# Performance work log

Hardware: AMD Instinct MI355X
Metric: run time of the kernel (lower is better)

The kernel has to match this reference:

```python
import jax, jax.numpy as jnp
import numpy as np

GAMMA = 0.5
NUM_ITER = 5


def setup_inputs() -> dict:
    key = jax.random.key(0)
    k1, k2 = jax.random.split(key)
    V, L = 10242, 42
    def_idxs = jax.random.uniform(k1, (V, L), dtype=jnp.float32, minval=1e-4, maxval=1.0)
    def_cont_ico_crf = jax.random.normal(k2, (V, 3), dtype=jnp.float32)
    # learned parameters, initialized as in the module
    filter_weights = jnp.ones((V, V), dtype=jnp.float32)
    spatial_weights = 4.0 * jnp.eye(V, dtype=jnp.float32)
    comp_matrix = jnp.eye(L, dtype=jnp.float32)
    return {
        "def_idxs": def_idxs,
        "def_cont_ico_crf": def_cont_ico_crf,
        "filter_weights": filter_weights,
        "spatial_weights": spatial_weights,
        "comp_matrix": comp_matrix,
    }


def reference(def_idxs, def_cont_ico_crf, filter_weights, spatial_weights, comp_matrix):
    V = def_cont_ico_crf.shape[0]
    # pairwise squared L2 distances between control points: [V, V]
    sq = jnp.sum(def_cont_ico_crf * def_cont_ico_crf, axis=1)
    d2 = sq[:, None] + sq[None, :] - 2.0 * (def_cont_ico_crf @ def_cont_ico_crf.T)
    smooth_filter = jnp.exp(-d2 / (2.0 * GAMMA ** 2))
    idx = jnp.arange(V)
    smooth_filter = smooth_filter.at[idx, idx].set(0.0)  # fill_diagonal_(0)

    U = jnp.log(jnp.clip(def_idxs, 1e-06, 1.0))  # unary potentials [V, L]
    q = jax.nn.softmax(U, axis=1)
    filter_mat = filter_weights * smooth_filter

    for _ in range(NUM_ITER):
        phi_t = filter_mat @ q                      # message passing [V, L]
        phi = -(spatial_weights @ phi_t)            # spatial reweighting
        phi = phi @ comp_matrix                     # label compatibility
        q = jax.nn.softmax(U - phi, axis=1)
    return q
```

## Files before the change

kernel.cpp:

```cpp
#include <hip/hip_runtime.h>
#include <stdint.h>

#define Vn 10242
#define Ln 42
#define LPn 48
#define VPn 10496
#define RBn 41
#define JPAD 10368
#define NITER 5
#define SCL 1.69864360f
#define BR 128

typedef float4 f4;
typedef short bf16x8 __attribute__((ext_vector_type(8)));
typedef float f32x4 __attribute__((ext_vector_type(4)));

__device__ __forceinline__ unsigned cvtpk_bf16(float a, float b) {
    unsigned r;
    asm("v_cvt_pk_bf16_f32 %0, %1, %2" : "=v"(r) : "v"(a), "v"(b));
    return r;
}
__device__ __forceinline__ unsigned short f2bf_rne(float f) {
    unsigned u = __float_as_uint(f);
    u = (u + 0x7fffu + ((u >> 16) & 1u)) >> 16;
    return (unsigned short)u;
}
__device__ __forceinline__ float bf2f(unsigned short h) {
    return __uint_as_float(((unsigned)h) << 16);
}

__global__ __launch_bounds__(256) void k_detect(const float* __restrict__ F,
                                                const float* __restrict__ S,
                                                int* flags, float* __restrict__ diagS) {
    int jj = blockIdx.x * 256 + threadIdx.x;
    if (jj >= Vn / 2) return;
    int j = jj * 2;
    const float c0 = F[0];
    int violF = 0, violS = 0;
    for (int i = blockIdx.y; i < Vn; i += (int)gridDim.y) {
        size_t off = (size_t)i * Vn + j;
        float2 f = *(const float2*)(F + off);
        float2 s = *(const float2*)(S + off);
        violF |= (f.x != c0) | (f.y != c0);
        if (i == j)          { diagS[j] = s.x;     violS |= (s.y != 0.0f); }
        else if (i == j + 1) { diagS[j + 1] = s.y; violS |= (s.x != 0.0f); }
        else                 violS |= (s.x != 0.0f) | (s.y != 0.0f);
    }
    if (violF) atomicOr(&flags[0], 1);
    if (violS) atomicOr(&flags[1], 1);
}

__global__ void k_detC(const float* __restrict__ Cm, int* flags) {
    int viol = 0;
    for (int idx = threadIdx.x; idx < Ln * Ln; idx += 256) {
        int r = idx / Ln, c = idx - r * Ln;
        float expct = (r == c) ? 1.0f : 0.0f;
        viol |= (Cm[idx] != expct);
    }
    if (viol) atomicOr(&flags[3], 1);
}

__global__ __launch_bounds__(256) void k_initU(const float* __restrict__ didx,
                                               const float* __restrict__ coords,
                                               float* __restrict__ U, float* __restrict__ qA,
                                               float* __restrict__ qB,
                                               unsigned short* __restrict__ qTAh,
                                               unsigned short* __restrict__ qTAl,
                                               unsigned short* __restrict__ qTBh,
                                               unsigned short* __restrict__ qTBl,
                                               float* __restrict__ xyz) {
    int row = blockIdx.x * 256 + threadIdx.x;
    if (row >= Vn) {
        #pragma unroll
        for (int l = 0; l < LPn; ++l) {
            U[(size_t)row * LPn + l] = 0.0f;
            qA[(size_t)row * LPn + l] = 0.0f;
            qB[(size_t)row * LPn + l] = 0.0f;
            qTAh[(size_t)l * VPn + row] = 0;
            qTAl[(size_t)l * VPn + row] = 0;
            qTBh[(size_t)l * VPn + row] = 0;
            qTBl[(size_t)l * VPn + row] = 0;
        }
        *(f4*)(xyz + (size_t)row * 4) = make_float4(0.f, 0.f, 0.f, 0.f);
        return;
    }
    float ux = SCL * coords[(size_t)row * 3 + 0];
    float uy = SCL * coords[(size_t)row * 3 + 1];
    float uz = SCL * coords[(size_t)row * 3 + 2];
    float ss = ux * ux + uy * uy + uz * uz;
    *(f4*)(xyz + (size_t)row * 4) = make_float4(ux, uy, uz, ss);
    float u[Ln];
    float mx = -3.0e38f;
    #pragma unroll
    for (int l = 0; l < Ln; ++l) {
        float x = didx[(size_t)row * Ln + l];
        x = fminf(fmaxf(x, 1e-6f), 1.0f);
        u[l] = __logf(x);
        mx = fmaxf(mx, u[l]);
    }
    float s = 0.0f;
    float e[Ln];
    #pragma unroll
    for (int l = 0; l < Ln; ++l) { e[l] = __expf(u[l] - mx); s += e[l]; }
    float inv = 1.0f / s;
    #pragma unroll
    for (int l = 0; l < Ln; ++l) {
        float qv = e[l] * inv;
        unsigned short h = f2bf_rne(qv);
        U[(size_t)row * LPn + l] = u[l];
        qA[(size_t)row * LPn + l] = qv;
        qTAh[(size_t)l * VPn + row] = h;
        qTAl[(size_t)l * VPn + row] = f2bf_rne(qv - bf2f(h));
    }
    #pragma unroll
    for (int l = Ln; l < LPn; ++l) {
        U[(size_t)row * LPn + l] = 0.0f;
        qA[(size_t)row * LPn + l] = 0.0f;
        qB[(size_t)row * LPn + l] = 0.0f;
        qTAh[(size_t)l * VPn + row] = 0;
        qTAl[(size_t)l * VPn + row] = 0;
        qTBh[(size_t)l * VPn + row] = 0;
        qTBl[(size_t)l * VPn + row] = 0;
    }
}

__global__ __launch_bounds__(256, 3) void k_phi_f(const unsigned short* __restrict__ qTh,
                                                  const unsigned short* __restrict__ qTl,
                                                  const f4* __restrict__ xyz4,
                                                  float* __restrict__ part,
                                                  const int* __restrict__ flags, int jchunk) {
    if (flags[0]) return;
    __shared__ uint4 Ah[8][BR];
    __shared__ uint4 Al[8][BR];
    __shared__ uint4 Bh[LPn][8];
    __shared__ uint4 Bl[LPn][8];
    const int t = threadIdx.x;
    const int lane = t & 63;
    const int wv = t >> 6;
    const int lo16 = lane & 15, hi4 = lane >> 4;
    const int rowbase = blockIdx.x * BR;
    f4 p0 = xyz4[rowbase + lane];
    f4 p1 = xyz4[rowbase + lane + 64];
    const float v0x = 2.f * p0.x, v0y = 2.f * p0.y, v0z = 2.f * p0.z, ns0 = -p0.w;
    const float v1x = 2.f * p1.x, v1y = 2.f * p1.y, v1z = 2.f * p1.z, ns1 = -p1.w;
    f32x4 acc[2][3];
    #pragma unroll
    for (int rs = 0; rs < 2; ++rs)
        #pragma unroll
        for (int cs = 0; cs < 3; ++cs) acc[rs][cs] = (f32x4){0.f, 0.f, 0.f, 0.f};
    const int j0 = blockIdx.y * jchunk;
    int j1 = j0 + jchunk; if (j1 > JPAD) j1 = JPAD;
    const int n0 = t >> 3, sl0 = t & 7;
    const int s1 = t + 256;
    const int n1 = s1 >> 3, sl1 = s1 & 7;
    const bool has1 = (s1 < LPn * 8);
    for (int jt = j0; jt < j1; jt += 64) {
        uint4 bh0 = *(const uint4*)(qTh + (size_t)n0 * VPn + jt + sl0 * 8);
        uint4 bl0 = *(const uint4*)(qTl + (size_t)n0 * VPn + jt + sl0 * 8);
        uint4 bh1, bl1;
        if (has1) {
            bh1 = *(const uint4*)(qTh + (size_t)n1 * VPn + jt + sl1 * 8);
            bl1 = *(const uint4*)(qTl + (size_t)n1 * VPn + jt + sl1 * 8);
        }
        const int jb = __builtin_amdgcn_readfirstlane(jt + wv * 16);
        unsigned ph0[8], ph1[8], pl0[8], pl1[8];
        #pragma unroll
        for (int m = 0; m < 16; m += 2) {
            f4 qa = xyz4[jb + m];
            f4 qb = xyz4[jb + m + 1];
            float wa0 = exp2f(fmaf(v0z, qa.z, fmaf(v0y, qa.y, fmaf(v0x, qa.x, ns0 - qa.w))));
            float wb0 = exp2f(fmaf(v0z, qb.z, fmaf(v0y, qb.y, fmaf(v0x, qb.x, ns0 - qb.w))));
            float wa1 = exp2f(fmaf(v1z, qa.z, fmaf(v1y, qa.y, fmaf(v1x, qa.x, ns1 - qa.w))));
            float wb1 = exp2f(fmaf(v1z, qb.z, fmaf(v1y, qb.y, fmaf(v1x, qb.x, ns1 - qb.w))));
            unsigned h0 = cvtpk_bf16(wa0, wb0);
            unsigned h1 = cvtpk_bf16(wa1, wb1);
            ph0[m >> 1] = h0;
            ph1[m >> 1] = h1;
            pl0[m >> 1] = cvtpk_bf16(wa0 - __uint_as_float(h0 << 16),
                                     wb0 - __uint_as_float(h0 & 0xffff0000u));
            pl1[m >> 1] = cvtpk_bf16(wa1 - __uint_as_float(h1 << 16),
                                     wb1 - __uint_as_float(h1 & 0xffff0000u));
        }
        __syncthreads();
        Ah[2 * wv][lane]          = make_uint4(ph0[0], ph0[1], ph0[2], ph0[3]);
        Ah[2 * wv + 1][lane]      = make_uint4(ph0[4], ph0[5], ph0[6], ph0[7]);
        Ah[2 * wv][lane + 64]     = make_uint4(ph1[0], ph1[1], ph1[2], ph1[3]);
        Ah[2 * wv + 1][lane + 64] = make_uint4(ph1[4], ph1[5], ph1[6], ph1[7]);
        Al[2 * wv][lane]          = make_uint4(pl0[0], pl0[1], pl0[2], pl0[3]);
        Al[2 * wv + 1][lane]      = make_uint4(pl0[4], pl0[5], pl0[6], pl0[7]);
        Al[2 * wv][lane + 64]     = make_uint4(pl1[0], pl1[1], pl1[2], pl1[3]);
        Al[2 * wv + 1][lane + 64] = make_uint4(pl1[4], pl1[5], pl1[6], pl1[7]);
        Bh[n0][sl0 ^ (n0 & 7)] = bh0;
        Bl[n0][sl0 ^ (n0 & 7)] = bl0;
        if (has1) {
            Bh[n1][sl1 ^ (n1 & 7)] = bh1;
            Bl[n1][sl1 ^ (n1 & 7)] = bl1;
        }
        __syncthreads();
        #pragma unroll
        for (int kk = 0; kk < 2; ++kk) {
            bf16x8 a0h = *(bf16x8*)&Ah[kk * 4 + hi4][wv * 32 + lo16];
            bf16x8 a1h = *(bf16x8*)&Ah[kk * 4 + hi4][wv * 32 + 16 + lo16];
            bf16x8 a0l = *(bf16x8*)&Al[kk * 4 + hi4][wv * 32 + lo16];
            bf16x8 a1l = *(bf16x8*)&Al[kk * 4 + hi4][wv * 32 + 16 + lo16];
            #pragma unroll
            for (int cs = 0; cs < 3; ++cs) {
                int n = cs * 16 + lo16;
                int slot = (kk * 4 + hi4) ^ (n & 7);
                bf16x8 bh = *(bf16x8*)&Bh[n][slot];
                bf16x8 bl = *(bf16x8*)&Bl[n][slot];
                acc[0][cs] = __builtin_amdgcn_mfma_f32_16x16x32_bf16(a0h, bh, acc[0][cs], 0, 0, 0);
                acc[0][cs] = __builtin_amdgcn_mfma_f32_16x16x32_bf16(a0h, bl, acc[0][cs], 0, 0, 0);
                acc[0][cs] = __builtin_amdgcn_mfma_f32_16x16x32_bf16(a0l, bh, acc[0][cs], 0, 0, 0);
                acc[0][cs] = __builtin_amdgcn_mfma_f32_16x16x32_bf16(a0l, bl, acc[0][cs], 0, 0, 0);
                acc[1][cs] = __builtin_amdgcn_mfma_f32_16x16x32_bf16(a1h, bh, acc[1][cs], 0, 0, 0);
                acc[1][cs] = __builtin_amdgcn_mfma_f32_16x16x32_bf16(a1h, bl, acc[1][cs], 0, 0, 0);
                acc[1][cs] = __builtin_amdgcn_mfma_f32_16x16x32_bf16(a1l, bh, acc[1][cs], 0, 0, 0);
                acc[1][cs] = __builtin_amdgcn_mfma_f32_16x16x32_bf16(a1l, bl, acc[1][cs], 0, 0, 0);
            }
        }
    }
    size_t pb = (size_t)blockIdx.y * LPn * VPn;
    #pragma unroll
    for (int rs = 0; rs < 2; ++rs)
        #pragma unroll
        for (int cs = 0; cs < 3; ++cs) {
            int col = cs * 16 + lo16;
            int row = rowbase + wv * 32 + rs * 16 + hi4 * 4;
            *(f4*)(part + pb + (size_t)col * VPn + row) =
                make_float4(acc[rs][cs][0], acc[rs][cs][1], acc[rs][cs][2], acc[rs][cs][3]);
        }
}

template <int USEG>
__device__ __forceinline__ void mat_gen_body(const float* __restrict__ W,
                                             const float* __restrict__ X,
                                             const float* __restrict__ xyz,
                                             float* __restrict__ part, int jchunk) {
    __shared__ float ldsW[256][33];
    int t = threadIdx.x;
    int row = blockIdx.x * 256 + t;
    bool act = (row < Vn);
    int j0 = blockIdx.y * jchunk;
    int j1 = j0 + jchunk; if (j1 > Vn) j1 = Vn;
    f4 xi = make_float4(0.f, 0.f, 0.f, 0.f);
    if (USEG && act) xi = *(const f4*)(xyz + (size_t)row * 4);
    f4 acc[12];
    #pragma unroll
    for (int c = 0; c < 12; ++c) acc[c] = make_float4(0.f, 0.f, 0.f, 0.f);
    for (int jt = j0; jt < j1; jt += 32) {
        __syncthreads();
        #pragma unroll
        for (int k = 0; k < 8; ++k) {
            int idx = t + k * 256;
            int r = idx >> 3;
            int cc = (idx & 7) << 2;
            int rr = blockIdx.x * 256 + r;
            int jc = jt + cc;
            float v0 = 0.f, v1 = 0.f, v2 = 0.f, v3 = 0.f;
            if (rr < Vn) {
                const float* wp = W + (size_t)rr * Vn + jc;
                if (jc + 0 < Vn) v0 = wp[0];
                if (jc + 1 < Vn) v1 = wp[1];
                if (jc + 2 < Vn) v2 = wp[2];
                if (jc + 3 < Vn) v3 = wp[3];
            }
            ldsW[r][cc + 0] = v0; ldsW[r][cc + 1] = v1;
            ldsW[r][cc + 2] = v2; ldsW[r][cc + 3] = v3;
        }
        __syncthreads();
        int jend = j1 - jt; if (jend > 32) jend = 32;
        for (int jj = 0; jj < jend; ++jj) {
            int j = jt + jj;
            float f = ldsW[t][jj];
            if (USEG) {
                f4 xj = *(const f4*)(xyz + (size_t)j * 4);
                float dx = xi.x - xj.x, dy = xi.y - xj.y, dz = xi.z - xj.z;
                float t2 = dx * dx; t2 = fmaf(dy, dy, t2); t2 = fmaf(dz, dz, t2);
                float w = exp2f(-t2);
                w = (j == row) ? 0.0f : w;
                f *= w;
            }
            const f4* qr = (const f4*)(X + (size_t)j * LPn);
            #pragma unroll
            for (int c = 0; c < 12; ++c) {
                f4 qv = qr[c];
                acc[c].x = fmaf(f, qv.x, acc[c].x);
                acc[c].y = fmaf(f, qv.y, acc[c].y);
                acc[c].z = fmaf(f, qv.z, acc[c].z);
                acc[c].w = fmaf(f, qv.w, acc[c].w);
            }
        }
    }
    size_t base = (size_t)blockIdx.y * LPn * VPn + row;
    if (act) {
        #pragma unroll
        for (int c = 0; c < 12; ++c) {
            part[base + (size_t)(4 * c + 0) * VPn] = acc[c].x;
            part[base + (size_t)(4 * c + 1) * VPn] = acc[c].y;
            part[base + (size_t)(4 * c + 2) * VPn] = acc[c].z;
            part[base + (size_t)(4 * c + 3) * VPn] = acc[c].w;
        }
    } else if (row < VPn) {
        #pragma unroll
        for (int c = 0; c < LPn; ++c) part[base + (size_t)c * VPn] = 0.0f;
    }
}

__global__ __launch_bounds__(256) void k_phi_g(const float* __restrict__ W,
                                               const float* __restrict__ q,
                                               const float* __restrict__ xyz,
                                               float* __restrict__ part,
                                               const int* __restrict__ flags, int jchunk) {
    if (!flags[0]) return;
    mat_gen_body<1>(W, q, xyz, part, jchunk);
}

__global__ __launch_bounds__(256) void k_sp(const float* __restrict__ Sw,
                                            const float* __restrict__ phi,
                                            float* __restrict__ part,
                                            const int* __restrict__ flags, int jchunk) {
    if (!flags[1]) return;
    mat_gen_body<0>(Sw, phi, (const float*)nullptr, part, jchunk);
}

__global__ __launch_bounds__(256) void k_R0(const float* __restrict__ part,
                                            const unsigned short* __restrict__ qTh,
                                            const unsigned short* __restrict__ qTl,
                                            float* __restrict__ phi,
                                            const int* __restrict__ flags,
                                            int NS, int gate) {
    if (gate && !flags[1]) return;
    int tg = blockIdx.x * 256 + threadIdx.x;
    int c = tg / (VPn / 4);
    int r4 = (tg - c * (VPn / 4)) * 4;
    f4 s = make_float4(0.f, 0.f, 0.f, 0.f);
    for (int n = 0; n < NS; ++n) {
        f4 v = *(const f4*)(part + ((size_t)n * LPn + c) * VPn + r4);
        s.x += v.x; s.y += v.y; s.z += v.z; s.w += v.w;
    }
    if (!gate && !flags[0]) {
        ushort4 h = *(const ushort4*)(qTh + (size_t)c * VPn + r4);
        ushort4 l = *(const ushort4*)(qTl + (size_t)c * VPn + r4);
        s.x -= bf2f(h.x) + bf2f(l.x);
        s.y -= bf2f(h.y) + bf2f(l.y);
        s.z -= bf2f(h.z) + bf2f(l.z);
        s.w -= bf2f(h.w) + bf2f(l.w);
    }
    phi[(size_t)(r4 + 0) * LPn + c] = s.x;
    phi[(size_t)(r4 + 1) * LPn + c] = s.y;
    phi[(size_t)(r4 + 2) * LPn + c] = s.z;
    phi[(size_t)(r4 + 3) * LPn + c] = s.w;
}

__global__ __launch_bounds__(256) void k_B(const float* __restrict__ U,
                                           const float* __restrict__ phi,
                                           const float* __restrict__ phi2,
                                           const float* __restrict__ diagS,
                                           const float* __restrict__ Cm,
                                           const float* __restrict__ Fw,
                                           const int* __restrict__ flags,
                                           float* __restrict__ qn,
                                           unsigned short* __restrict__ qTnh,
                                           unsigned short* __restrict__ qTnl,
                                           float* __restrict__ outp, int last) {
    __shared__ float ldsC[Ln][LPn];
    int t = threadIdx.x;
    if (flags[3]) {
        for (int idx = t; idx < Ln * LPn; idx += 256) {
            int m = idx / LPn, l = idx - m * LPn;
            ldsC[m][l] = (l < Ln) ? Cm[(size_t)m * Ln + l] : 0.0f;
        }
    }
    __syncthreads();
    int row = blockIdx.x * 256 + t;
    if (row >= Vn) return;
    const float* src = flags[1] ? phi2 : phi;
    float pt[LPn];
    #pragma unroll
    for (int c = 0; c < 12; ++c) {
        f4 v = *(const f4*)(src + (size_t)row * LPn + 4 * c);
        pt[4 * c + 0] = v.x; pt[4 * c + 1] = v.y;
        pt[4 * c + 2] = v.z; pt[4 * c + 3] = v.w;
    }
    float scale = (flags[0] ? 1.0f : Fw[0]) * (flags[1] ? 1.0f : diagS[row]);
    float ph[LPn];
    if (flags[3]) {
        #pragma unroll
        for (int c = 0; c < LPn; ++c) ph[c] = 0.f;
        #pragma unroll
        for (int m = 0; m < Ln; ++m) {
            float pm = pt[m];
            #pragma unroll
            for (int c = 0; c < 12; ++c) {
                f4 cv = *(const f4*)&ldsC[m][4 * c];
                ph[4 * c + 0] = fmaf(pm, cv.x, ph[4 * c + 0]);
                ph[4 * c + 1] = fmaf(pm, cv.y, ph[4 * c + 1]);
                ph[4 * c + 2] = fmaf(pm, cv.z, ph[4 * c + 2]);
                ph[4 * c + 3] = fmaf(pm, cv.w, ph[4 * c + 3]);
            }
        }
    } else {
        #pragma unroll
        for (int c = 0; c < LPn; ++c) ph[c] = pt[c];
    }
    float lg[LPn];
    #pragma unroll
    for (int c = 0; c < 12; ++c) {
        f4 uv = *(const f4*)(U + (size_t)row * LPn + 4 * c);
        lg[4 * c + 0] = uv.x + scale * ph[4 * c + 0];
        lg[4 * c + 1] = uv.y + scale * ph[4 * c + 1];
        lg[4 * c + 2] = uv.z + scale * ph[4 * c + 2];
        lg[4 * c + 3] = uv.w + scale * ph[4 * c + 3];
    }
    float mx = lg[0];
    #pragma unroll
    for (int l = 1; l < Ln; ++l) mx = fmaxf(mx, lg[l]);
    float s = 0.f;
    float e[LPn];
    #pragma unroll
    for (int l = 0; l < Ln; ++l) { e[l] = __expf(lg[l] - mx); s += e[l]; }
    #pragma unroll
    for (int l = Ln; l < LPn; ++l) e[l] = 0.f;
    float inv = 1.0f / s;
    #pragma unroll
    for (int c = 0; c < 12; ++c) {
        f4 v = make_float4(e[4 * c + 0] * inv, e[4 * c + 1] * inv,
                           e[4 * c + 2] * inv, e[4 * c + 3] * inv);
        *(f4*)(qn + (size_t)row * LPn + 4 * c) = v;
    }
    #pragma unroll
    for (int l = 0; l < Ln; ++l) {
        float qv = e[l] * inv;
        unsigned short h = f2bf_rne(qv);
        qTnh[(size_t)l * VPn + row] = h;
        qTnl[(size_t)l * VPn + row] = f2bf_rne(qv - bf2f(h));
    }
    if (last) {
        #pragma unroll
        for (int l = 0; l < Ln; ++l) outp[(size_t)row * Ln + l] = e[l] * inv;
    }
}

extern "C" void kernel_launch(void* const* d_in, const int* in_sizes, int n_in,
                              void* d_out, int out_size, void* d_ws, size_t ws_size,
                              hipStream_t stream) {
    const float* didx   = (const float*)d_in[0];
    const float* coords = (const float*)d_in[1];
    const float* Fw     = (const float*)d_in[2];
    const float* Sw     = (const float*)d_in[3];
    const float* Cm     = (const float*)d_in[4];
    float* outp = (float*)d_out;
    float* wsf = (float*)d_ws;

    int*   flags = (int*)wsf;
    float* diagS = wsf + 16;
    float* xyz   = diagS + VPn;
    float* U     = xyz + (size_t)VPn * 4;
    float* qA    = U + (size_t)VPn * LPn;
    float* qB    = qA + (size_t)VPn * LPn;
    float* phi   = qB + (size_t)VPn * LPn;
    float* phi2  = phi + (size_t)VPn * LPn;
    unsigned short* qTAh = (unsigned short*)(phi2 + (size_t)VPn * LPn);
    unsigned short* qTAl = qTAh + (size_t)LPn * VPn;
    unsigned short* qTBh = qTAl + (size_t)LPn * VPn;
    unsigned short* qTBl = qTBh + (size_t)LPn * VPn;
    float* part  = (float*)(qTBl + (size_t)LPn * VPn);

    size_t base_f = 16 + (size_t)VPn * (1 + 4) + (size_t)VPn * LPn * 5 + (size_t)VPn * LPn * 2;
    int NS = 8;
    while (NS > 1 && (base_f + (size_t)NS * LPn * VPn) * 4 > ws_size) NS >>= 1;
    int jchunkF = ((JPAD / 64 + NS - 1) / NS) * 64;
    int jchunkG = (((Vn + NS - 1) / NS) + 31) & ~31;

    hipMemsetAsync(flags, 0, 16, stream);
    hipLaunchKernelGGL(k_detect, dim3((Vn / 2 + 255) / 256, 1024), dim3(256), 0, stream,
                       Fw, Sw, flags, diagS);
    hipLaunchKernelGGL(k_detC, dim3(1), dim3(256), 0, stream, Cm, flags);
    hipLaunchKernelGGL(k_initU, dim3(RBn), dim3(256), 0, stream,
                       didx, coords, U, qA, qB, qTAh, qTAl, qTBh, qTBl, xyz);

    float* qcur = qA;  float* qnxt = qB;
    unsigned short* qThc = qTAh;  unsigned short* qTlc = qTAl;
    unsigned short* qThn = qTBh;  unsigned short* qTln = qTBl;
    for (int it = 0; it < NITER; ++it) {
        hipLaunchKernelGGL(k_phi_f, dim3(VPn / BR, NS), dim3(256), 0, stream,
                           qThc, qTlc, (const f4*)xyz, part, flags, jchunkF);
        hipLaunchKernelGGL(k_phi_g, dim3(RBn, NS), dim3(256), 0, stream,
                           Fw, qcur, xyz, part, flags, jchunkG);
        hipLaunchKernelGGL(k_R0, dim3(LPn * (VPn / 4) / 256), dim3(256), 0, stream,
                           part, qThc, qTlc, phi, flags, NS, 0);
        hipLaunchKernelGGL(k_sp, dim3(RBn, NS), dim3(256), 0, stream,
                           Sw, phi, part, flags, jchunkG);
        hipLaunchKernelGGL(k_R0, dim3(LPn * (VPn / 4) / 256), dim3(256), 0, stream,
                           part, qThc, qTlc, phi2, flags, NS, 1);
        hipLaunchKernelGGL(k_B, dim3(RBn), dim3(256), 0, stream,
                           U, phi, phi2, diagS, Cm, Fw, flags, qnxt, qThn, qTln, outp,
                           (it == NITER - 1) ? 1 : 0);
        float* tq = qcur; qcur = qnxt; qnxt = tq;
        unsigned short* th = qThc; qThc = qThn; qThn = th;
        unsigned short* tl = qTlc; qTlc = qTln; qTln = tl;
    }
}
```

Before: 653.5 us.

## Compute filter weights directly in MFMA register layout, drop LDS staging

Rewrites the fast-path message-passing kernel so each lane computes the Gaussian weights for exactly the A-operand fragment it feeds to the MFMA. This removes the shared-memory staging and both block barriers, and B operands are loaded straight from global memory. It also drops the low*low bf16 correction term (3 MFMAs per pair instead of 4), raises occupancy to 4 blocks per CU, and allows up to 12 j-splits. The cost is lost B-operand sharing across waves, which means more global/L2 traffic. It also carries a small precision loss from the dropped correction term.

```diff
diff --git a/kernel.cpp b/kernel.cpp
--- a/kernel.cpp
+++ b/kernel.cpp
@@ -14,6 +14,7 @@
 typedef float4 f4;
 typedef short bf16x8 __attribute__((ext_vector_type(8)));
 typedef float f32x4 __attribute__((ext_vector_type(4)));
+typedef unsigned u32x4 __attribute__((ext_vector_type(4)));
 
 __device__ __forceinline__ unsigned cvtpk_bf16(float a, float b) {
     unsigned r;
@@ -124,25 +125,23 @@
     }
 }
 
-__global__ __launch_bounds__(256, 3) void k_phi_f(const unsigned short* __restrict__ qTh,
+__global__ __launch_bounds__(256, 4) void k_phi_r(const unsigned short* __restrict__ qTh,
                                                   const unsigned short* __restrict__ qTl,
                                                   const f4* __restrict__ xyz4,
                                                   float* __restrict__ part,
                                                   const int* __restrict__ flags, int jchunk) {
     if (flags[0]) return;
-    __shared__ uint4 Ah[8][BR];
-    __shared__ uint4 Al[8][BR];
-    __shared__ uint4 Bh[LPn][8];
-    __shared__ uint4 Bl[LPn][8];
     const int t = threadIdx.x;
     const int lane = t & 63;
     const int wv = t >> 6;
     const int lo16 = lane & 15, hi4 = lane >> 4;
     const int rowbase = blockIdx.x * BR;
-    f4 p0 = xyz4[rowbase + lane];
-    f4 p1 = xyz4[rowbase + lane + 64];
-    const float v0x = 2.f * p0.x, v0y = 2.f * p0.y, v0z = 2.f * p0.z, ns0 = -p0.w;
-    const float v1x = 2.f * p1.x, v1y = 2.f * p1.y, v1z = 2.f * p1.z, ns1 = -p1.w;
+    const int i0 = rowbase + wv * 32 + lo16;
+    const int i1 = i0 + 16;
+    f4 p0 = xyz4[i0];
+    f4 p1 = xyz4[i1];
+    const float a0x = 2.f * p0.x, a0y = 2.f * p0.y, a0z = 2.f * p0.z, c0 = -p0.w;
+    const float a1x = 2.f * p1.x, a1y = 2.f * p1.y, a1z = 2.f * p1.z, c1 = -p1.w;
     f32x4 acc[2][3];
     #pragma unroll
     for (int rs = 0; rs < 2; ++rs)
@@ -150,74 +149,43 @@
         for (int cs = 0; cs < 3; ++cs) acc[rs][cs] = (f32x4){0.f, 0.f, 0.f, 0.f};
     const int j0 = blockIdx.y * jchunk;
     int j1 = j0 + jchunk; if (j1 > JPAD) j1 = JPAD;
-    const int n0 = t >> 3, sl0 = t & 7;
-    const int s1 = t + 256;
-    const int n1 = s1 >> 3, sl1 = s1 & 7;
-    const bool has1 = (s1 < LPn * 8);
-    for (int jt = j0; jt < j1; jt += 64) {
-        uint4 bh0 = *(const uint4*)(qTh + (size_t)n0 * VPn + jt + sl0 * 8);
-        uint4 bl0 = *(const uint4*)(qTl + (size_t)n0 * VPn + jt + sl0 * 8);
-        uint4 bh1, bl1;
-        if (has1) {
-            bh1 = *(const uint4*)(qTh + (size_t)n1 * VPn + jt + sl1 * 8);
-            bl1 = *(const uint4*)(qTl + (size_t)n1 * VPn + jt + sl1 * 8);
-        }
-        const int jb = __builtin_amdgcn_readfirstlane(jt + wv * 16);
-        unsigned ph0[8], ph1[8], pl0[8], pl1[8];
-        #pragma unroll
-        for (int m = 0; m < 16; m += 2) {
-            f4 qa = xyz4[jb + m];
-            f4 qb = xyz4[jb + m + 1];
-            float wa0 = exp2f(fmaf(v0z, qa.z, fmaf(v0y, qa.y, fmaf(v0x, qa.x, ns0 - qa.w))));
-            float wb0 = exp2f(fmaf(v0z, qb.z, fmaf(v0y, qb.y, fmaf(v0x, qb.x, ns0 - qb.w))));
-            float wa1 = exp2f(fmaf(v1z, qa.z, fmaf(v1y, qa.y, fmaf(v1x, qa.x, ns1 - qa.w))));
-            float wb1 = exp2f(fmaf(v1z, qb.z, fmaf(v1y, qb.y, fmaf(v1x, qb.x, ns1 - qb.w))));
-            unsigned h0 = cvtpk_bf16(wa0, wb0);
-            unsigned h1 = cvtpk_bf16(wa1, wb1);
-            ph0[m >> 1] = h0;
-            ph1[m >> 1] = h1;
-            pl0[m >> 1] = cvtpk_bf16(wa0 - __uint_as_float(h0 << 16),
-                                     wb0 - __uint_as_float(h0 & 0xffff0000u));
-            pl1[m >> 1] = cvtpk_bf16(wa1 - __uint_as_float(h1 << 16),
-                                     wb1 - __uint_as_float(h1 & 0xffff0000u));
-        }
-        __syncthreads();
-        Ah[2 * wv][lane]          = make_uint4(ph0[0], ph0[1], ph0[2], ph0[3]);
-        Ah[2 * wv + 1][lane]      = make_uint4(ph0[4], ph0[5], ph0[6], ph0[7]);
-        Ah[2 * wv][lane + 64]     = make_uint4(ph1[0], ph1[1], ph1[2], ph1[3]);
-        Ah[2 * wv + 1][lane + 64] = make_uint4(ph1[4], ph1[5], ph1[6], ph1[7]);
-        Al[2 * wv][lane]          = make_uint4(pl0[0], pl0[1], pl0[2], pl0[3]);
-        Al[2 * wv + 1][lane]      = make_uint4(pl0[4], pl0[5], pl0[6], pl0[7]);
-        Al[2 * wv][lane + 64]     = make_uint4(pl1[0], pl1[1], pl1[2], pl1[3]);
-        Al[2 * wv + 1][lane + 64] = make_uint4(pl1[4], pl1[5], pl1[6], pl1[7]);
-        Bh[n0][sl0 ^ (n0 & 7)] = bh0;
-        Bl[n0][sl0 ^ (n0 & 7)] = bl0;
-        if (has1) {
-            Bh[n1][sl1 ^ (n1 & 7)] = bh1;
-            Bl[n1][sl1 ^ (n1 & 7)] = bl1;
-        }
-        __syncthreads();
-        #pragma unroll
-        for (int kk = 0; kk < 2; ++kk) {
-            bf16x8 a0h = *(bf16x8*)&Ah[kk * 4 + hi4][wv * 32 + lo16];
-            bf16x8 a1h = *(bf16x8*)&Ah[kk * 4 + hi4][wv * 32 + 16 + lo16];
-            bf16x8 a0l = *(bf16x8*)&Al[kk * 4 + hi4][wv * 32 + lo16];
-            bf16x8 a1l = *(bf16x8*)&Al[kk * 4 + hi4][wv * 32 + 16 + lo16];
-            #pragma unroll
-            for (int cs = 0; cs < 3; ++cs) {
-                int n = cs * 16 + lo16;
-                int slot = (kk * 4 + hi4) ^ (n & 7);
-                bf16x8 bh = *(bf16x8*)&Bh[n][slot];
-                bf16x8 bl = *(bf16x8*)&Bl[n][slot];
-                acc[0][cs] = __builtin_amdgcn_mfma_f32_16x16x32_bf16(a0h, bh, acc[0][cs], 0, 0, 0);
-                acc[0][cs] = __builtin_amdgcn_mfma_f32_16x16x32_bf16(a0h, bl, acc[0][cs], 0, 0, 0);
-                acc[0][cs] = __builtin_amdgcn_mfma_f32_16x16x32_bf16(a0l, bh, acc[0][cs], 0, 0, 0);
-                acc[0][cs] = __builtin_amdgcn_mfma_f32_16x16x32_bf16(a0l, bl, acc[0][cs], 0, 0, 0);
-                acc[1][cs] = __builtin_amdgcn_mfma_f32_16x16x32_bf16(a1h, bh, acc[1][cs], 0, 0, 0);
-                acc[1][cs] = __builtin_amdgcn_mfma_f32_16x16x32_bf16(a1h, bl, acc[1][cs], 0, 0, 0);
-                acc[1][cs] = __builtin_amdgcn_mfma_f32_16x16x32_bf16(a1l, bh, acc[1][cs], 0, 0, 0);
-                acc[1][cs] = __builtin_amdgcn_mfma_f32_16x16x32_bf16(a1l, bl, acc[1][cs], 0, 0, 0);
-            }
+    for (int jt = j0; jt < j1; jt += 32) {
+        const int jb = jt + hi4 * 8;
+        float w0[8], w1[8];
+        #pragma unroll
+        for (int m = 0; m < 8; ++m) {
+            f4 xj = xyz4[jb + m];
+            w0[m] = exp2f(fmaf(a0z, xj.z, fmaf(a0y, xj.y, fmaf(a0x, xj.x, c0 - xj.w))));
+            w1[m] = exp2f(fmaf(a1z, xj.z, fmaf(a1y, xj.y, fmaf(a1x, xj.x, c1 - xj.w))));
+        }
+        unsigned h0[4], h1[4], l0[4], l1[4];
+        #pragma unroll
+        for (int m = 0; m < 4; ++m) {
+            unsigned hh0 = cvtpk_bf16(w0[2 * m], w0[2 * m + 1]);
+            unsigned hh1 = cvtpk_bf16(w1[2 * m], w1[2 * m + 1]);
+            h0[m] = hh0; h1[m] = hh1;
+            l0[m] = cvtpk_bf16(w0[2 * m]     - __uint_as_float(hh0 << 16),
+                               w0[2 * m + 1] - __uint_as_float(hh0 & 0xffff0000u));
+            l1[m] = cvtpk_bf16(w1[2 * m]     - __uint_as_float(hh1 << 16),
+                               w1[2 * m + 1] - __uint_as_float(hh1 & 0xffff0000u));
+        }
+        union Uu { u32x4 u; bf16x8 v; };
+        Uu A0h, A0l, A1h, A1l;
+        A0h.u = (u32x4){h0[0], h0[1], h0[2], h0[3]};
+        A0l.u = (u32x4){l0[0], l0[1], l0[2], l0[3]};
+        A1h.u = (u32x4){h1[0], h1[1], h1[2], h1[3]};
+        A1l.u = (u32x4){l1[0], l1[1], l1[2], l1[3]};
+        #pragma unroll
+        for (int cs = 0; cs < 3; ++cs) {
+            const size_t bo = (size_t)(cs * 16 + lo16) * VPn + jb;
+            bf16x8 bh = *(const bf16x8*)(qTh + bo);
+            bf16x8 bl = *(const bf16x8*)(qTl + bo);
+            acc[0][cs] = __builtin_amdgcn_mfma_f32_16x16x32_bf16(A0h.v, bh, acc[0][cs], 0, 0, 0);
+            acc[0][cs] = __builtin_amdgcn_mfma_f32_16x16x32_bf16(A0h.v, bl, acc[0][cs], 0, 0, 0);
+            acc[0][cs] = __builtin_amdgcn_mfma_f32_16x16x32_bf16(A0l.v, bh, acc[0][cs], 0, 0, 0);
+            acc[1][cs] = __builtin_amdgcn_mfma_f32_16x16x32_bf16(A1h.v, bh, acc[1][cs], 0, 0, 0);
+            acc[1][cs] = __builtin_amdgcn_mfma_f32_16x16x32_bf16(A1h.v, bl, acc[1][cs], 0, 0, 0);
+            acc[1][cs] = __builtin_amdgcn_mfma_f32_16x16x32_bf16(A1l.v, bh, acc[1][cs], 0, 0, 0);
         }
     }
     size_t pb = (size_t)blockIdx.y * LPn * VPn;
@@ -468,9 +436,9 @@
     float* part  = (float*)(qTBl + (size_t)LPn * VPn);
 
     size_t base_f = 16 + (size_t)VPn * (1 + 4) + (size_t)VPn * LPn * 5 + (size_t)VPn * LPn * 2;
-    int NS = 8;
-    while (NS > 1 && (base_f + (size_t)NS * LPn * VPn) * 4 > ws_size) NS >>= 1;
-    int jchunkF = ((JPAD / 64 + NS - 1) / NS) * 64;
+    int NS = 12;
+    while (NS > 1 && (base_f + (size_t)NS * LPn * VPn) * 4 > ws_size) NS--;
+    int jchunkF = (((JPAD / 64) + NS - 1) / NS) * 64;
     int jchunkG = (((Vn + NS - 1) / NS) + 31) & ~31;
 
     hipMemsetAsync(flags, 0, 16, stream);
@@ -484,7 +452,7 @@
     unsigned short* qThc = qTAh;  unsigned short* qTlc = qTAl;
     unsigned short* qThn = qTBh;  unsigned short* qTln = qTBl;
     for (int it = 0; it < NITER; ++it) {
-        hipLaunchKernelGGL(k_phi_f, dim3(VPn / BR, NS), dim3(256), 0, stream,
+        hipLaunchKernelGGL(k_phi_r, dim3(VPn / BR, NS), dim3(256), 0, stream,
                            qThc, qTlc, (const f4*)xyz, part, flags, jchunkF);
         hipLaunchKernelGGL(k_phi_g, dim3(RBn, NS), dim3(256), 0, stream,
                            Fw, qcur, xyz, part, flags, jchunkG);
```

New measurement: 803.7 us. 23.0% more time.
